# Kernel tuning notes

Hardware: AMD Instinct MI355X
Metric: run time of the kernel (lower is better)

## Reference

```python
import jax, jax.numpy as jnp
import numpy as np

T, B, V, D, H = 1024, 128, 50257, 128, 512


def _lstm_cell(x, h, c, w_ih, w_hh, b_ih, b_hh):
    # x: [B, D], h/c: [B, H]; gates: [B, 4H] in PyTorch i,f,g,o order
    gates = x @ w_ih.T + h @ w_hh.T + b_ih + b_hh
    i, f, g, o = jnp.split(gates, 4, axis=-1)
    c_new = jax.nn.sigmoid(f) * c + jax.nn.sigmoid(i) * jnp.tanh(g)
    h_new = jax.nn.sigmoid(o) * jnp.tanh(c_new)
    return h_new, c_new


def setup_inputs() -> dict:
    key = jax.random.key(0)
    ks = jax.random.split(key, 7)
    s = 1.0 / np.sqrt(H)
    return {
        "input_ids": jax.random.randint(ks[0], (T, B), 0, V),
        "seq_len": jnp.sort(jax.random.randint(ks[1], (B,), 0, T)),
        "emb_weight": jax.random.normal(ks[2], (V, D), jnp.float32) * 0.1,
        "w_ih": jax.random.uniform(ks[3], (4 * H, D), jnp.float32, -s, s),
        "w_hh": jax.random.uniform(ks[4], (4 * H, H), jnp.float32, -s, s),
        "b_ih": jax.random.uniform(ks[5], (4 * H,), jnp.float32, -s, s),
        "b_hh": jax.random.uniform(ks[6], (4 * H,), jnp.float32, -s, s),
    }


def reference(input_ids, seq_len, emb_weight, w_ih, w_hh, b_ih, b_hh):
    Tn, Bn = input_ids.shape
    Hn = w_hh.shape[1]
    dt = emb_weight.dtype
    z = jnp.zeros((Bn, Hn), dt)

    def step(carry, inp):
        h, c, last_h, last_c = carry
        t, ids = inp
        x = emb_weight[ids]                       # embedding lookup (dropout=identity, eval)
        h_new, c_new = _lstm_cell(x, h, c, w_ih, w_hh, b_ih, b_hh)
        # hold previously reported features once timestep >= seq_len (skip blend at t==0)
        hold = ((t > 0) & (t >= seq_len)).astype(dt)[:, None]
        blend_c = c_new * (1.0 - hold) + last_c * hold
        blend_h = h_new * (1.0 - hold) + last_h * hold
        # RNN internal state keeps evolving (module is stateful across steps)
        return (h_new, c_new, blend_h, blend_c), None

    (_, _, _, final_c), _ = jax.lax.scan(
        step, (z, z, z, z), (jnp.arange(Tn), input_ids)
    )
    return final_c  # [B, H] mask-blended last cell state
```

## Files before the change

kernel.cpp:

```cpp
#include <hip/hip_runtime.h>

typedef _Float16 half8 __attribute__((ext_vector_type(8)));
typedef float float4v __attribute__((ext_vector_type(4)));
typedef unsigned long long u64;

#define TSEQ  1024
#define BATCH 128
#define HID   512
#define DIN   128

#define HW_STRIDE 264
#define HBUF_WORDS (8 * HW_STRIDE)
#define GOFF (2 * HBUF_WORDS * 4)
#define PUB_OFF (GOFF + 4 * 8 * 32 * 4)
#define LDS_BYTES (PUB_OFF + 512)

#define WS_H16_OFF  0
#define WS_BAR_OFF  (2 * BATCH * HID * 2)
#define WS_XALL_OFF (1u << 20)
#define WS_NEED     ((size_t)WS_XALL_OFF + (size_t)TSEQ * BATCH * DIN * 2)

__device__ inline half8 cvt8(float4v a, float4v b) {
    half8 r;
    r[0] = (_Float16)a[0]; r[1] = (_Float16)a[1];
    r[2] = (_Float16)a[2]; r[3] = (_Float16)a[3];
    r[4] = (_Float16)b[0]; r[5] = (_Float16)b[1];
    r[6] = (_Float16)b[2]; r[7] = (_Float16)b[3];
    return r;
}

__device__ inline float sigm(float x) {
    return __builtin_amdgcn_rcpf(1.0f + __builtin_amdgcn_exp2f(-1.44269504f * x));
}
__device__ inline float tanh_fast(float x) { return 2.0f * sigm(2.0f * x) - 1.0f; }

template <bool XA>
__global__ __launch_bounds__(256, 1)
void lstm_persistent(const int* __restrict__ ids,
                     const int* __restrict__ seq_len,
                     const float* __restrict__ emb,
                     const float* __restrict__ w_ih,
                     const float* __restrict__ w_hh,
                     const float* __restrict__ b_ih,
                     const float* __restrict__ b_hh,
                     float* __restrict__ out,
                     _Float16* __restrict__ h16,
                     _Float16* __restrict__ x_all,
                     int* __restrict__ bar)
{
    __shared__ __align__(16) char smem[LDS_BYTES];
    unsigned* hsu = (unsigned*)smem;
    _Float16* hsh = (_Float16*)smem;
    float*    gs  = (float*)(smem + GOFF);
    unsigned short* pub = (unsigned short*)(smem + PUB_OFF);

    const int tid  = threadIdx.x;
    const int lane = tid & 63;
    const int wv   = tid >> 6;
    const int team = blockIdx.x & 15;
    const int p    = blockIdx.x >> 4;
    const int rowbase   = team * 8;
    const int unit_base = p * 32 + wv * 8;

    const int col  = lane & 15;
    const int kq   = lane >> 4;
    const int arow = lane & 7;
    const int my_row  = lane >> 3;
    const int my_unit = unit_base + (lane & 7);

    if (XA) {
        for (int pair = blockIdx.x * 256 + tid; pair < TSEQ * BATCH;
             pair += 256 * 256) {
            const float* src = emb + (size_t)ids[pair] * DIN;
            _Float16* dst = x_all + (size_t)pair * DIN;
#pragma unroll
            for (int k = 0; k < 16; ++k) {
                float4v a = *(const float4v*)(src + k * 8);
                float4v c = *(const float4v*)(src + k * 8 + 4);
                *(half8*)(dst + k * 8) = cvt8(a, c);
            }
        }
        __threadfence();
        __syncthreads();
        if (tid == 0) {
            __hip_atomic_fetch_add(bar, 1, __ATOMIC_RELEASE,
                                   __HIP_MEMORY_SCOPE_AGENT);
            int g = 0;
            while (__hip_atomic_load(bar, __ATOMIC_ACQUIRE,
                                     __HIP_MEMORY_SCOPE_AGENT) < 256
                   && ++g < (1 << 26)) { }
        }
        __syncthreads();
        __threadfence();
    }

    int tmax = 0, my_tstar = 0;
    for (int r = 0; r < 8; ++r) {
        int s  = seq_len[rowbase + r];
        int ts = (s > 0) ? (s - 1) : 0;
        if (r == my_row) my_tstar = ts;
        tmax = (ts > tmax) ? ts : tmax;
    }

    const int wrow0 = (col & 3) * HID + unit_base + (col >> 2);
    const int wrow1 = (col & 3) * HID + unit_base + 4 + (col >> 2);
    const float bias0 = b_ih[wrow0] + b_hh[wrow0];
    const float bias1 = b_ih[wrow1] + b_hh[wrow1];

    half8 whhf0[16], whhf1[16];
#pragma unroll
    for (int kt = 0; kt < 16; ++kt) {
        const float* s0 = w_hh + (size_t)wrow0 * HID + kt * 32 + kq * 8;
        const float* s1 = w_hh + (size_t)wrow1 * HID + kt * 32 + kq * 8;
        whhf0[kt] = cvt8(*(const float4v*)s0, *(const float4v*)(s0 + 4));
        whhf1[kt] = cvt8(*(const float4v*)s1, *(const float4v*)(s1 + 4));
    }
    half8 wihf0[4], wihf1[4];
#pragma unroll
    for (int kt = 0; kt < 4; ++kt) {
        const float* s0 = w_ih + (size_t)wrow0 * DIN + kt * 32 + kq * 8;
        const float* s1 = w_ih + (size_t)wrow1 * DIN + kt * 32 + kq * 8;
        wihf0[kt] = cvt8(*(const float4v*)s0, *(const float4v*)(s0 + 4));
        wihf1[kt] = cvt8(*(const float4v*)s1, *(const float4v*)(s1 + 4));
    }

    float c_state = 0.0f;
    const int crow = tid >> 5;
    const int coff = tid & 31;

    half8 xf[4], xn[4];
    if (XA) {
        const _Float16* x0 = x_all + ((size_t)0 * BATCH + rowbase + arow) * DIN;
        const int t1 = (tmax > 0) ? 1 : 0;
        const _Float16* x1 = x_all + ((size_t)t1 * BATCH + rowbase + arow) * DIN;
#pragma unroll
        for (int kt = 0; kt < 4; ++kt) {
            xf[kt] = *(const half8*)(x0 + kt * 32 + kq * 8);
            xn[kt] = *(const half8*)(x1 + kt * 32 + kq * 8);
        }
    } else {
        const int id0 = ids[rowbase + arow];
        const float* xrow = emb + (size_t)id0 * DIN;
#pragma unroll
        for (int kt = 0; kt < 4; ++kt) {
            const float* s = xrow + kt * 32 + kq * 8;
            xf[kt] = cvt8(*(const float4v*)s, *(const float4v*)(s + 4));
        }
    }

    float4v a0 = {bias0, bias0, bias0, bias0}, b0 = {0,0,0,0}, c0 = {0,0,0,0}, d0 = {0,0,0,0};
    float4v a1 = {bias1, bias1, bias1, bias1}, b1 = {0,0,0,0}, c1 = {0,0,0,0}, d1 = {0,0,0,0};
    a0 = __builtin_amdgcn_mfma_f32_16x16x32_f16(xf[0], wihf0[0], a0, 0, 0, 0);
    b0 = __builtin_amdgcn_mfma_f32_16x16x32_f16(xf[1], wihf0[1], b0, 0, 0, 0);
    c0 = __builtin_amdgcn_mfma_f32_16x16x32_f16(xf[2], wihf0[2], c0, 0, 0, 0);
    d0 = __builtin_amdgcn_mfma_f32_16x16x32_f16(xf[3], wihf0[3], d0, 0, 0, 0);
    a1 = __builtin_amdgcn_mfma_f32_16x16x32_f16(xf[0], wihf1[0], a1, 0, 0, 0);
    b1 = __builtin_amdgcn_mfma_f32_16x16x32_f16(xf[1], wihf1[1], b1, 0, 0, 0);
    c1 = __builtin_amdgcn_mfma_f32_16x16x32_f16(xf[2], wihf1[2], c1, 0, 0, 0);
    d1 = __builtin_amdgcn_mfma_f32_16x16x32_f16(xf[3], wihf1[3], d1, 0, 0, 0);

    const u64 LSBM = 0x0001000100010001ull;

    for (int t = 0; t <= tmax; ++t) {
        const int bs = t & 1;
        int id_next = 0;
        if (!XA) {
            const int tn = (t < tmax) ? (t + 1) : t;
            id_next = ids[tn * BATCH + rowbase + arow];
        }

        if (t > 0) {
            const u64* rowp = (const u64*)(h16
                + (size_t)((t + 1) & 1) * BATCH * HID + (rowbase + crow) * HID);
            const u64 want = ((((t - 1) >> 1) & 1) ^ 1) ? LSBM : 0ull;
            unsigned* dstw = hsu + bs * HBUF_WORDS + crow * HW_STRIDE + 2 * coff;
            u64 v[4];
            unsigned pending = 0xF;
#pragma unroll
            for (int j = 0; j < 4; ++j)
                v[j] = __hip_atomic_load(rowp + coff + 32 * j,
                                         __ATOMIC_RELAXED, __HIP_MEMORY_SCOPE_AGENT);
#pragma unroll
            for (int j = 0; j < 4; ++j) {
                if (((v[j] ^ want) & LSBM) == 0) {
                    *(u64*)(dstw + 64 * j) = v[j];
                    pending &= ~(1u << j);
                }
            }
            int round = 0, guard = 0;
            while (pending) {
#pragma unroll
                for (int j = 0; j < 4; ++j) {
                    if (pending & (1u << j)) {
                        u64 x = __hip_atomic_load(rowp + coff + 32 * j,
                                                  __ATOMIC_RELAXED,
                                                  __HIP_MEMORY_SCOPE_AGENT);
                        if (((x ^ want) & LSBM) == 0) {
                            *(u64*)(dstw + 64 * j) = x;
                            pending &= ~(1u << j);
                        }
                    }
                }
                if (!pending) break;
                if (++round >= 3) __builtin_amdgcn_s_sleep(1);
                if (++guard > (1 << 20)) break;
            }
        }
        __syncthreads();

        float4v xraw[8];
        if (!XA) {
            const float* xrow = emb + (size_t)id_next * DIN;
#pragma unroll
            for (int kt = 0; kt < 4; ++kt) {
                xraw[2 * kt]     = *(const float4v*)(xrow + kt * 32 + kq * 8);
                xraw[2 * kt + 1] = *(const float4v*)(xrow + kt * 32 + kq * 8 + 4);
            }
        }

        if (t > 0) {
            const _Float16* hb = hsh + bs * HBUF_WORDS * 2;
#pragma unroll
            for (int kt = 0; kt < 16; ++kt) {
                half8 af = *(const half8*)(hb + arow * (HW_STRIDE * 2) + kt * 32 + kq * 8);
                switch (kt & 3) {
                case 0:
                    a0 = __builtin_amdgcn_mfma_f32_16x16x32_f16(af, whhf0[kt], a0, 0, 0, 0);
                    a1 = __builtin_amdgcn_mfma_f32_16x16x32_f16(af, whhf1[kt], a1, 0, 0, 0);
                    break;
                case 1:
                    b0 = __builtin_amdgcn_mfma_f32_16x16x32_f16(af, whhf0[kt], b0, 0, 0, 0);
                    b1 = __builtin_amdgcn_mfma_f32_16x16x32_f16(af, whhf1[kt], b1, 0, 0, 0);
                    break;
                case 2:
                    c0 = __builtin_amdgcn_mfma_f32_16x16x32_f16(af, whhf0[kt], c0, 0, 0, 0);
                    c1 = __builtin_amdgcn_mfma_f32_16x16x32_f16(af, whhf1[kt], c1, 0, 0, 0);
                    break;
                default:
                    d0 = __builtin_amdgcn_mfma_f32_16x16x32_f16(af, whhf0[kt], d0, 0, 0, 0);
                    d1 = __builtin_amdgcn_mfma_f32_16x16x32_f16(af, whhf1[kt], d1, 0, 0, 0);
                }
            }
        }
        const float4v g0 = (a0 + b0) + (c0 + d0);
        const float4v g1 = (a1 + b1) + (c1 + d1);

        float* gw = gs + wv * 256;
        if (lane < 32) {
            const int grow = (lane >> 4) * 4;
#pragma unroll
            for (int r = 0; r < 4; ++r) {
                gw[(grow + r) * 32 + col]      = g0[r];
                gw[(grow + r) * 32 + 16 + col] = g1[r];
            }
        }
        const float4v g4 = *(const float4v*)(gw + my_row * 32 + (lane & 7) * 4);

        const float i_s = sigm(g4[0]);
        const float f_s = sigm(g4[1]);
        const float g_t = tanh_fast(g4[2]);
        const float o_s = sigm(g4[3]);
        c_state = f_s * c_state + i_s * g_t;
        const float hn = o_s * tanh_fast(c_state);

        if (t == my_tstar)
            out[(rowbase + my_row) * HID + my_unit] = c_state;

        {
            const unsigned pub_phase = (((unsigned)t >> 1) & 1u) ^ 1u;
            unsigned short hb16 = __builtin_bit_cast(unsigned short, (_Float16)hn);
            hb16 = (unsigned short)((hb16 & 0xFFFEu) | pub_phase);
            pub[my_row * 32 + wv * 8 + (lane & 7)] = hb16;
        }
        __syncthreads();
        if (tid < 64) {
            const int r = tid >> 3, seg = tid & 7;
            const u64 pk = *(const u64*)(pub + r * 32 + seg * 4);
            __hip_atomic_store((u64*)((unsigned short*)h16
                                   + (size_t)(t & 1) * BATCH * HID
                                   + (rowbase + r) * HID + p * 32) + seg,
                               pk, __ATOMIC_RELAXED, __HIP_MEMORY_SCOPE_AGENT);
        }

        if (XA) {
#pragma unroll
            for (int kt = 0; kt < 4; ++kt) xf[kt] = xn[kt];
            const int t2 = (t + 2 <= tmax) ? (t + 2) : tmax;
            const _Float16* xs2 = x_all + ((size_t)t2 * BATCH + rowbase + arow) * DIN;
#pragma unroll
            for (int kt = 0; kt < 4; ++kt)
                xn[kt] = *(const half8*)(xs2 + kt * 32 + kq * 8);
        } else {
#pragma unroll
            for (int kt = 0; kt < 4; ++kt)
                xf[kt] = cvt8(xraw[2 * kt], xraw[2 * kt + 1]);
        }

        a0 = (float4v){bias0, bias0, bias0, bias0}; b0 = (float4v){0,0,0,0};
        c0 = (float4v){0,0,0,0};                    d0 = (float4v){0,0,0,0};
        a1 = (float4v){bias1, bias1, bias1, bias1}; b1 = (float4v){0,0,0,0};
        c1 = (float4v){0,0,0,0};                    d1 = (float4v){0,0,0,0};
        a0 = __builtin_amdgcn_mfma_f32_16x16x32_f16(xf[0], wihf0[0], a0, 0, 0, 0);
        b0 = __builtin_amdgcn_mfma_f32_16x16x32_f16(xf[1], wihf0[1], b0, 0, 0, 0);
        c0 = __builtin_amdgcn_mfma_f32_16x16x32_f16(xf[2], wihf0[2], c0, 0, 0, 0);
        d0 = __builtin_amdgcn_mfma_f32_16x16x32_f16(xf[3], wihf0[3], d0, 0, 0, 0);
        a1 = __builtin_amdgcn_mfma_f32_16x16x32_f16(xf[0], wihf1[0], a1, 0, 0, 0);
        b1 = __builtin_amdgcn_mfma_f32_16x16x32_f16(xf[1], wihf1[1], b1, 0, 0, 0);
        c1 = __builtin_amdgcn_mfma_f32_16x16x32_f16(xf[2], wihf1[2], c1, 0, 0, 0);
        d1 = __builtin_amdgcn_mfma_f32_16x16x32_f16(xf[3], wihf1[3], d1, 0, 0, 0);

        __builtin_amdgcn_s_sleep(6);
    }
}

extern "C" void kernel_launch(void* const* d_in, const int* in_sizes, int n_in,
                              void* d_out, int out_size, void* d_ws, size_t ws_size,
                              hipStream_t stream)
{
    const int*   ids  = (const int*)d_in[0];
    const int*   slen = (const int*)d_in[1];
    const float* emb  = (const float*)d_in[2];
    const float* wih  = (const float*)d_in[3];
    const float* whh  = (const float*)d_in[4];
    const float* bih  = (const float*)d_in[5];
    const float* bhh  = (const float*)d_in[6];
    float* out = (float*)d_out;

    _Float16* h16   = (_Float16*)((char*)d_ws + WS_H16_OFF);
    int*      bar   = (int*)((char*)d_ws + WS_BAR_OFF);
    _Float16* x_all = (_Float16*)((char*)d_ws + WS_XALL_OFF);

    if (ws_size >= WS_NEED) {
        hipMemsetAsync(bar, 0, sizeof(int), stream);
        hipLaunchKernelGGL((lstm_persistent<true>), dim3(256), dim3(256), 0, stream,
                           ids, slen, emb, wih, whh, bih, bhh, out,
                           h16, x_all, bar);
    } else {
        hipLaunchKernelGGL((lstm_persistent<false>), dim3(256), dim3(256), 0, stream,
                           ids, slen, emb, wih, whh, bih, bhh, out,
                           h16, x_all, bar);
    }
}
```

Measured before the change: 1.854 ms.

## Split hidden-state wait into halves to overlap second-half polling with MFMA

The cross-block wait for the previous step's hidden state is split into two halves. The block waits only for the first half of the K dimension before the first barrier, runs the first eight recurrent MFMA k-tiles, then finishes polling the second half, hits a second barrier, and runs the remaining tiles. This is meant to hide part of the inter-workgroup synchronisation latency behind compute on the serial recurrence. In exchange it adds an extra __syncthreads per timestep and more code on the critical path.

```diff
diff --git a/kernel.cpp b/kernel.cpp
--- a/kernel.cpp
+++ b/kernel.cpp
@@ -169,13 +169,16 @@
             id_next = ids[tn * BATCH + rowbase + arow];
         }
 
+        const u64* rowp = (const u64*)(h16
+            + (size_t)((t + 1) & 1) * BATCH * HID + (rowbase + crow) * HID);
+        const u64 want = ((((t - 1) >> 1) & 1) ^ 1) ? LSBM : 0ull;
+        unsigned* dstw = hsu + bs * HBUF_WORDS + crow * HW_STRIDE + 2 * coff;
+        unsigned pending = 0;
+        u64 vB[2];
+
         if (t > 0) {
-            const u64* rowp = (const u64*)(h16
-                + (size_t)((t + 1) & 1) * BATCH * HID + (rowbase + crow) * HID);
-            const u64 want = ((((t - 1) >> 1) & 1) ^ 1) ? LSBM : 0ull;
-            unsigned* dstw = hsu + bs * HBUF_WORDS + crow * HW_STRIDE + 2 * coff;
+            pending = 0xF;
             u64 v[4];
-            unsigned pending = 0xF;
 #pragma unroll
             for (int j = 0; j < 4; ++j)
                 v[j] = __hip_atomic_load(rowp + coff + 32 * j,
@@ -188,9 +191,9 @@
                 }
             }
             int round = 0, guard = 0;
-            while (pending) {
-#pragma unroll
-                for (int j = 0; j < 4; ++j) {
+            while (pending & 0x3u) {
+#pragma unroll
+                for (int j = 0; j < 2; ++j) {
                     if (pending & (1u << j)) {
                         u64 x = __hip_atomic_load(rowp + coff + 32 * j,
                                                   __ATOMIC_RELAXED,
@@ -201,7 +204,7 @@
                         }
                     }
                 }
-                if (!pending) break;
+                if (!(pending & 0x3u)) break;
                 if (++round >= 3) __builtin_amdgcn_s_sleep(1);
                 if (++guard > (1 << 20)) break;
             }
@@ -218,10 +221,73 @@
             }
         }
 
+        if (t > 0 && (pending & 0x4u))
+            vB[0] = __hip_atomic_load(rowp + coff + 64,
+                                      __ATOMIC_RELAXED, __HIP_MEMORY_SCOPE_AGENT);
+        if (t > 0 && (pending & 0x8u))
+            vB[1] = __hip_atomic_load(rowp + coff + 96,
+                                      __ATOMIC_RELAXED, __HIP_MEMORY_SCOPE_AGENT);
+
         if (t > 0) {
             const _Float16* hb = hsh + bs * HBUF_WORDS * 2;
 #pragma unroll
-            for (int kt = 0; kt < 16; ++kt) {
+            for (int kt = 0; kt < 8; ++kt) {
+                half8 af = *(const half8*)(hb + arow * (HW_STRIDE * 2) + kt * 32 + kq * 8);
+                switch (kt & 3) {
+                case 0:
+                    a0 = __builtin_amdgcn_mfma_f32_16x16x32_f16(af, whhf0[kt], a0, 0, 0, 0);
+                    a1 = __builtin_amdgcn_mfma_f32_16x16x32_f16(af, whhf1[kt], a1, 0, 0, 0);
+                    break;
+                case 1:
+                    b0 = __builtin_amdgcn_mfma_f32_16x16x32_f16(af, whhf0[kt], b0, 0, 0, 0);
+                    b1 = __builtin_amdgcn_mfma_f32_16x16x32_f16(af, whhf1[kt], b1, 0, 0, 0);
+                    break;
+                case 2:
+                    c0 = __builtin_amdgcn_mfma_f32_16x16x32_f16(af, whhf0[kt], c0, 0, 0, 0);
+                    c1 = __builtin_amdgcn_mfma_f32_16x16x32_f16(af, whhf1[kt], c1, 0, 0, 0);
+                    break;
+                default:
+                    d0 = __builtin_amdgcn_mfma_f32_16x16x32_f16(af, whhf0[kt], d0, 0, 0, 0);
+                    d1 = __builtin_amdgcn_mfma_f32_16x16x32_f16(af, whhf1[kt], d1, 0, 0, 0);
+                }
+            }
+            if (pending & 0xCu) {
+#pragma unroll
+                for (int j = 2; j < 4; ++j) {
+                    if (pending & (1u << j)) {
+                        const u64 x = vB[j - 2];
+                        if (((x ^ want) & LSBM) == 0) {
+                            *(u64*)(dstw + 64 * j) = x;
+                            pending &= ~(1u << j);
+                        }
+                    }
+                }
+                int round = 0, guard = 0;
+                while (pending & 0xCu) {
+#pragma unroll
+                    for (int j = 2; j < 4; ++j) {
+                        if (pending & (1u << j)) {
+                            u64 x = __hip_atomic_load(rowp + coff + 32 * j,
+                                                      __ATOMIC_RELAXED,
+                                                      __HIP_MEMORY_SCOPE_AGENT);
+                            if (((x ^ want) & LSBM) == 0) {
+                                *(u64*)(dstw + 64 * j) = x;
+                                pending &= ~(1u << j);
+                            }
+                        }
+                    }
+                    if (!(pending & 0xCu)) break;
+                    if (++round >= 3) __builtin_amdgcn_s_sleep(1);
+                    if (++guard > (1 << 20)) break;
+                }
+            }
+        }
+        __syncthreads();
+
+        if (t > 0) {
+            const _Float16* hb = hsh + bs * HBUF_WORDS * 2;
+#pragma unroll
+            for (int kt = 8; kt < 16; ++kt) {
                 half8 af = *(const half8*)(hb + arow * (HW_STRIDE * 2) + kt * 32 + kq * 8);
                 switch (kt & 3) {
                 case 0:
```

Result: slower. 2.146 ms (+15.8%).
